# Kernel tuning notes

Measured on AMD Instinct MI355X. Metric: run time of the kernel, lower is better.

The kernel has to match this reference:

```python
import jax, jax.numpy as jnp
import numpy as np

N_NODES = 100000
N_EDGES = 1600000
N_GRAPHS = 1024
HID = 128
FINAL = 128
SPATIAL = 3
NUM_LAYERS = 3
VOCAB = 100


def _linear_params(key, d_in, d_out):
    k1, k2 = jax.random.split(key)
    s = 1.0 / np.sqrt(d_in)
    W = jax.random.uniform(k1, (d_out, d_in), jnp.float32, -s, s)
    b = jax.random.uniform(k2, (d_out,), jnp.float32, -s, s)
    return W, b


def setup_inputs() -> dict:
    key = jax.random.key(0)
    ks = jax.random.split(key, 16)
    z = jax.random.randint(ks[0], (N_NODES,), 0, VOCAB)
    pos = jax.random.normal(ks[1], (N_NODES, SPATIAL), jnp.float32)
    edge_index = jax.random.randint(ks[2], (2, N_EDGES), 0, N_NODES)
    batch = jnp.sort(jax.random.randint(ks[3], (N_NODES,), 0, N_GRAPHS))
    emb_table = jax.random.normal(ks[4], (VOCAB, HID), jnp.float32)
    W_pos, b_pos = _linear_params(ks[5], SPATIAL, HID)
    W_comb, b_comb = _linear_params(ks[6], 2 * HID, HID)
    # GIN: each conv's MLP is Linear(d,d) -> ReLU -> Linear(d,d); all dims 128 here.
    gW1, gb1, gW2, gb2 = [], [], [], []
    for i in range(NUM_LAYERS):
        k = jax.random.fold_in(ks[7], i)
        ka, kb = jax.random.split(k)
        W1, b1 = _linear_params(ka, HID, HID)
        W2, b2 = _linear_params(kb, HID, FINAL if i == NUM_LAYERS - 1 else HID)
        gW1.append(W1); gb1.append(b1); gW2.append(W2); gb2.append(b2)
    gin_W1 = jnp.stack(gW1); gin_b1 = jnp.stack(gb1)
    gin_W2 = jnp.stack(gW2); gin_b2 = jnp.stack(gb2)
    W_p1, b_p1 = _linear_params(ks[8], FINAL, FINAL)
    W_p2, b_p2 = _linear_params(ks[9], FINAL, 1)
    return {
        "z": z, "pos": pos, "edge_index": edge_index, "batch": batch,
        "emb_table": emb_table, "W_pos": W_pos, "b_pos": b_pos,
        "W_comb": W_comb, "b_comb": b_comb,
        "gin_W1": gin_W1, "gin_b1": gin_b1, "gin_W2": gin_W2, "gin_b2": gin_b2,
        "W_p1": W_p1, "b_p1": b_p1, "W_p2": W_p2, "b_p2": b_p2,
    }


def reference(z, pos, edge_index, batch, emb_table, W_pos, b_pos, W_comb, b_comb,
              gin_W1, gin_b1, gin_W2, gin_b2, W_p1, b_p1, W_p2, b_p2):
    src, dst = edge_index[0], edge_index[1]
    # initial node embedding: embed(z) || linear(pos) -> linear -> relu
    atom = emb_table[z]                                   # [N, H]
    pe = pos @ W_pos.T + b_pos                            # [N, H]
    x = jax.nn.relu(jnp.concatenate([atom, pe], axis=-1) @ W_comb.T + b_comb)
    # GIN layers: x' = MLP((1+eps)*x + sum_{j->i} x_j), eps=0; act between convs only
    for i in range(NUM_LAYERS):
        aggr = jax.ops.segment_sum(x[src], dst, num_segments=N_NODES)  # [N, H]
        h = aggr + x
        h = jax.nn.relu(h @ gin_W1[i].T + gin_b1[i])
        x = h @ gin_W2[i].T + gin_b2[i]
        if i < NUM_LAYERS - 1:
            x = jax.nn.relu(x)
    # sum pooling per graph, then predict MLP
    g = jax.ops.segment_sum(x, batch, num_segments=N_GRAPHS)  # [G, F]
    h = jax.nn.relu(g @ W_p1.T + b_p1)
    return h @ W_p2.T + b_p2                              # [G, 1]
```

## Files before the change

kernel.cpp:

```cpp
#include <hip/hip_runtime.h>
#include <hip/hip_bf16.h>

#define HID 128
#define CAP 64

typedef __attribute__((ext_vector_type(8))) short bfrag;
typedef __attribute__((ext_vector_type(4))) float f32x4;

static inline size_t align256(size_t x) { return (x + 255) & ~(size_t)255; }

__device__ __forceinline__ unsigned short f2bf(float f) {
  unsigned int x = __float_as_uint(f);
  unsigned int r = x + 0x7fffu + ((x >> 16) & 1u);
  return (unsigned short)(r >> 16);
}
__device__ __forceinline__ float bflo(unsigned int u) { return __uint_as_float(u << 16); }
__device__ __forceinline__ float bfhi(unsigned int u) { return __uint_as_float(u & 0xffff0000u); }


#define NBK 2048

__global__ __launch_bounds__(256) void k_prep(const int* __restrict__ src,
                                              const int* __restrict__ dst,
                                              int* __restrict__ cnt,
                                              int* __restrict__ bsrc, int E, int N,
                                              const float* __restrict__ W_comb,
                                              const float* __restrict__ gW1,
                                              const float* __restrict__ gW2,
                                              unsigned short* __restrict__ Wcb,
                                              unsigned short* __restrict__ W1b,
                                              unsigned short* __restrict__ W2b,
                                              const int* __restrict__ batch,
                                              int* __restrict__ goff, int G) {
  const int bid = blockIdx.x;
  const int tid = threadIdx.x;
  if (bid < NBK) {
    const int slice = bid & 7;
    const int sidx = bid >> 3;
    const int s_lo = (int)(((long long)slice * N) >> 3);
    const int s_hi = (int)(((long long)(slice + 1) * N) >> 3);
    for (int e = sidx * 256 + tid; e < E; e += (NBK / 8) * 256) {
      int d = dst[e];
      if (d >= s_lo && d < s_hi) {
        int slot = atomicAdd(&cnt[d], 1);
        if (slot < CAP) bsrc[(size_t)d * CAP + slot] = src[e];
      }
    }
  } else if (bid < NBK + 192) {
    int i = (bid - NBK) * 256 + tid;
    if (i < 128 * 256) Wcb[i] = f2bf(W_comb[i]);
    if (i < 3 * 128 * 128) {
      W1b[i] = f2bf(gW1[i]);
      W2b[i] = f2bf(gW2[i]);
    }
  } else {
    int g = (bid - NBK - 192) * 256 + tid;
    if (g <= G) {
      int lo = 0, hi = N;
      while (lo < hi) {
        int mid = (lo + hi) >> 1;
        if (batch[mid] < g) lo = mid + 1; else hi = mid;
      }
      goff[g] = lo;
    }
  }
}


__global__ __launch_bounds__(256, 2) void k_init_mm(const int* __restrict__ z,
                                                    const float* __restrict__ pos,
                                                    const float* __restrict__ emb,
                                                    const float* __restrict__ W_pos,
                                                    const float* __restrict__ b_pos,
                                                    const unsigned short* __restrict__ Wcb,
                                                    const float* __restrict__ bias,
                                                    unsigned short* __restrict__ Y, int n) {
  __shared__ unsigned int sE[32 * 128];
  const int t = threadIdx.x;
  const int w = t >> 6;
  const int l = t & 63;
  const int lr = l & 15;
  const int lk = l >> 4;

  bfrag bfr[2][8];
#pragma unroll
  for (int s = 0; s < 2; ++s)
#pragma unroll
    for (int ks = 0; ks < 8; ++ks)
      bfr[s][ks] = *(const bfrag*)(Wcb + (size_t)(32 * w + 16 * s + lr) * 256 + ks * 32 + lk * 8);
  const float bias0 = bias[32 * w + lr];
  const float bias1 = bias[32 * w + 16 + lr];

  const int m0 = blockIdx.x * 32;
  {
    const int r = t >> 3, i = t & 7;
    int node = m0 + r;
    if (node >= n) node = n - 1;
    const int zz = z[node];
    const float p0 = pos[node * 3 + 0], p1 = pos[node * 3 + 1], p2 = pos[node * 3 + 2];
    const int swz = (r & 7) << 2;
#pragma unroll
    for (int k = 0; k < 16; ++k) {
      const int j = i + k * 8;
      float v0, v1;
      if (j < 64) {
        const float2 ev = *(const float2*)&emb[(size_t)zz * 128 + 2 * j];
        v0 = ev.x; v1 = ev.y;
      } else {
        const int f0 = 2 * j - 128;
        v0 = b_pos[f0] + W_pos[f0 * 3] * p0 + W_pos[f0 * 3 + 1] * p1 + W_pos[f0 * 3 + 2] * p2;
        v1 = b_pos[f0 + 1] + W_pos[f0 * 3 + 3] * p0 + W_pos[f0 * 3 + 4] * p1 +
             W_pos[f0 * 3 + 5] * p2;
      }
      sE[r * 128 + (j ^ swz)] = (unsigned int)f2bf(v0) | ((unsigned int)f2bf(v1) << 16);
    }
  }
  __syncthreads();

  f32x4 acc00 = {0.f, 0.f, 0.f, 0.f}, acc01 = acc00, acc10 = acc00, acc11 = acc00;
#pragma unroll
  for (int mt = 0; mt < 2; ++mt) {
    const int row = 16 * mt + lr;
    const int swz = (row & 7) << 2;
#pragma unroll
    for (int ks = 0; ks < 8; ++ks) {
      const bfrag a = *(const bfrag*)&sE[row * 128 + ((ks * 16 + lk * 4) ^ swz)];
      if (mt == 0) {
        acc00 = __builtin_amdgcn_mfma_f32_16x16x32_bf16(a, bfr[0][ks], acc00, 0, 0, 0);
        acc01 = __builtin_amdgcn_mfma_f32_16x16x32_bf16(a, bfr[1][ks], acc01, 0, 0, 0);
      } else {
        acc10 = __builtin_amdgcn_mfma_f32_16x16x32_bf16(a, bfr[0][ks], acc10, 0, 0, 0);
        acc11 = __builtin_amdgcn_mfma_f32_16x16x32_bf16(a, bfr[1][ks], acc11, 0, 0, 0);
      }
    }
  }

#pragma unroll
  for (int mt = 0; mt < 2; ++mt) {
#pragma unroll
    for (int s = 0; s < 2; ++s) {
      const f32x4 a = mt == 0 ? (s == 0 ? acc00 : acc01) : (s == 0 ? acc10 : acc11);
      const float bb = s == 0 ? bias0 : bias1;
      const int col = 32 * w + 16 * s + lr;
#pragma unroll
      for (int r = 0; r < 4; ++r) {
        const int row = m0 + 16 * mt + 4 * lk + r;
        if (row < n) Y[(size_t)row * HID + col] = f2bf(fmaxf(a[r] + bb, 0.f));
      }
    }
  }
}


__global__ __launch_bounds__(256, 2) void k_ag_mm(const unsigned int* __restrict__ X,
                                                  const int* __restrict__ cnt,
                                                  const int* __restrict__ bsrc,
                                                  const unsigned short* __restrict__ Wb,
                                                  const float* __restrict__ bias,
                                                  unsigned short* __restrict__ Y, int n) {
  __shared__ unsigned int sA[32 * 64];
  const int t = threadIdx.x;
  const int w = t >> 6;
  const int l = t & 63;
  const int lr = l & 15;
  const int lk = l >> 4;

  bfrag bfr[2][4];
#pragma unroll
  for (int s = 0; s < 2; ++s)
#pragma unroll
    for (int ks = 0; ks < 4; ++ks)
      bfr[s][ks] = *(const bfrag*)(Wb + (size_t)(32 * w + 16 * s + lr) * HID + ks * 32 + lk * 8);
  const float bias0 = bias[32 * w + lr];
  const float bias1 = bias[32 * w + 16 + lr];

  const int ntiles = (n + 31) >> 5;
  for (int tile = blockIdx.x; tile < ntiles; tile += gridDim.x) {
    const int m0 = tile * 32;
#pragma unroll
    for (int ri = 0; ri < 8; ++ri) {
      const int row = 8 * w + ri;
      int node = m0 + row;
      if (node >= n) node = n - 1;
      int deg = cnt[node];
      if (deg > CAP) deg = CAP;
      const int eidx = bsrc[(size_t)node * CAP + l];
      const unsigned int u = X[(size_t)node * 64 + l];
      float a0 = bflo(u), a1 = bfhi(u);
      float b0 = 0.f, b1 = 0.f, c0 = 0.f, c1 = 0.f, d0 = 0.f, d1 = 0.f;
      int k = 0;
      for (; k + 3 < deg; k += 4) {
        const int s0 = __shfl(eidx, k), s1 = __shfl(eidx, k + 1);
        const int s2 = __shfl(eidx, k + 2), s3 = __shfl(eidx, k + 3);
        const unsigned int ua = X[(size_t)s0 * 64 + l];
        const unsigned int ub = X[(size_t)s1 * 64 + l];
        const unsigned int uc = X[(size_t)s2 * 64 + l];
        const unsigned int ud = X[(size_t)s3 * 64 + l];
        a0 += bflo(ua); a1 += bfhi(ua);
        b0 += bflo(ub); b1 += bfhi(ub);
        c0 += bflo(uc); c1 += bfhi(uc);
        d0 += bflo(ud); d1 += bfhi(ud);
      }
      for (; k < deg; ++k) {
        const unsigned int ua = X[(size_t)__shfl(eidx, k) * 64 + l];
        a0 += bflo(ua); a1 += bfhi(ua);
      }
      const float r0 = (a0 + b0) + (c0 + d0);
      const float r1 = (a1 + b1) + (c1 + d1);
      sA[row * 64 + (l ^ ((row & 7) << 2))] =
          (unsigned int)f2bf(r0) | ((unsigned int)f2bf(r1) << 16);
    }
    __syncthreads();

    f32x4 acc00 = {0.f, 0.f, 0.f, 0.f}, acc01 = acc00, acc10 = acc00, acc11 = acc00;
#pragma unroll
    for (int mt = 0; mt < 2; ++mt) {
      const int row = 16 * mt + lr;
      const int swz = (row & 7) << 2;
#pragma unroll
      for (int ks = 0; ks < 4; ++ks) {
        const bfrag a = *(const bfrag*)&sA[row * 64 + ((ks * 16 + lk * 4) ^ swz)];
        if (mt == 0) {
          acc00 = __builtin_amdgcn_mfma_f32_16x16x32_bf16(a, bfr[0][ks], acc00, 0, 0, 0);
          acc01 = __builtin_amdgcn_mfma_f32_16x16x32_bf16(a, bfr[1][ks], acc01, 0, 0, 0);
        } else {
          acc10 = __builtin_amdgcn_mfma_f32_16x16x32_bf16(a, bfr[0][ks], acc10, 0, 0, 0);
          acc11 = __builtin_amdgcn_mfma_f32_16x16x32_bf16(a, bfr[1][ks], acc11, 0, 0, 0);
        }
      }
    }

#pragma unroll
    for (int mt = 0; mt < 2; ++mt) {
#pragma unroll
      for (int s = 0; s < 2; ++s) {
        const f32x4 a = mt == 0 ? (s == 0 ? acc00 : acc01) : (s == 0 ? acc10 : acc11);
        const float bb = s == 0 ? bias0 : bias1;
        const int col = 32 * w + 16 * s + lr;
#pragma unroll
        for (int r = 0; r < 4; ++r) {
          const int row = m0 + 16 * mt + 4 * lk + r;
          if (row < n) Y[(size_t)row * HID + col] = f2bf(fmaxf(a[r] + bb, 0.f));
        }
      }
    }
    __syncthreads();
  }
}


template <int RELU>
__global__ __launch_bounds__(256, 2) void k_mm2(const unsigned short* __restrict__ X,
                                                const unsigned short* __restrict__ Wb,
                                                const float* __restrict__ bias,
                                                unsigned short* __restrict__ Y, int M) {
  const int t = threadIdx.x;
  const int w = t >> 6;
  const int l = t & 63;
  const int lr = l & 15;
  const int lk = l >> 4;

  bfrag bfr[2][4];
#pragma unroll
  for (int s = 0; s < 2; ++s)
#pragma unroll
    for (int ks = 0; ks < 4; ++ks)
      bfr[s][ks] = *(const bfrag*)(Wb + (size_t)(32 * w + 16 * s + lr) * HID + ks * 32 + lk * 8);
  const float bias0 = bias[32 * w + lr];
  const float bias1 = bias[32 * w + 16 + lr];

  for (int m0 = blockIdx.x * 32; m0 < M; m0 += gridDim.x * 32) {
    bfrag afr[2][4];
#pragma unroll
    for (int mt = 0; mt < 2; ++mt)
#pragma unroll
      for (int ks = 0; ks < 4; ++ks)
        afr[mt][ks] = *(const bfrag*)(X + (size_t)(m0 + 16 * mt + lr) * HID + ks * 32 + lk * 8);

    f32x4 acc00 = {0.f, 0.f, 0.f, 0.f}, acc01 = acc00, acc10 = acc00, acc11 = acc00;
#pragma unroll
    for (int ks = 0; ks < 4; ++ks) {
      acc00 = __builtin_amdgcn_mfma_f32_16x16x32_bf16(afr[0][ks], bfr[0][ks], acc00, 0, 0, 0);
      acc01 = __builtin_amdgcn_mfma_f32_16x16x32_bf16(afr[0][ks], bfr[1][ks], acc01, 0, 0, 0);
      acc10 = __builtin_amdgcn_mfma_f32_16x16x32_bf16(afr[1][ks], bfr[0][ks], acc10, 0, 0, 0);
      acc11 = __builtin_amdgcn_mfma_f32_16x16x32_bf16(afr[1][ks], bfr[1][ks], acc11, 0, 0, 0);
    }

#pragma unroll
    for (int mt = 0; mt < 2; ++mt) {
#pragma unroll
      for (int s = 0; s < 2; ++s) {
        const f32x4 a = mt == 0 ? (s == 0 ? acc00 : acc01) : (s == 0 ? acc10 : acc11);
        const float bb = s == 0 ? bias0 : bias1;
        const int col = 32 * w + 16 * s + lr;
#pragma unroll
        for (int r = 0; r < 4; ++r) {
          const int row = m0 + 16 * mt + 4 * lk + r;
          float v = a[r] + bb;
          if (RELU) v = fmaxf(v, 0.f);
          if (row < M) Y[(size_t)row * HID + col] = f2bf(v);
        }
      }
    }
  }
}


__global__ __launch_bounds__(128) void k_pool(const unsigned short* __restrict__ X,
                                              const int* __restrict__ goff,
                                              const float* __restrict__ Wp1,
                                              const float* __restrict__ bp1,
                                              const float* __restrict__ Wp2,
                                              const float* __restrict__ bp2,
                                              float* __restrict__ out, int G) {
  __shared__ float sg[HID];
  __shared__ float sred[HID];
  int g = blockIdx.x;
  int f = threadIdx.x;
  int n0 = goff[g], n1 = goff[g + 1];
  float c0 = 0.f, c1 = 0.f, c2 = 0.f, c3 = 0.f;
  int nn = n0;
  for (; nn + 3 < n1; nn += 4) {
    c0 += __uint_as_float((unsigned int)X[(size_t)nn * HID + f] << 16);
    c1 += __uint_as_float((unsigned int)X[(size_t)(nn + 1) * HID + f] << 16);
    c2 += __uint_as_float((unsigned int)X[(size_t)(nn + 2) * HID + f] << 16);
    c3 += __uint_as_float((unsigned int)X[(size_t)(nn + 3) * HID + f] << 16);
  }
  for (; nn < n1; ++nn) c0 += __uint_as_float((unsigned int)X[(size_t)nn * HID + f] << 16);
  sg[f] = (c0 + c1) + (c2 + c3);
  __syncthreads();
  float a0 = 0.f, a1 = 0.f, a2 = 0.f, a3 = 0.f;
#pragma unroll
  for (int k4 = 0; k4 < 32; ++k4) {
    float4 wv = *(const float4*)&Wp1[f * HID + k4 * 4];
    float4 xv = *(const float4*)&sg[k4 * 4];
    a0 += wv.x * xv.x; a1 += wv.y * xv.y; a2 += wv.z * xv.z; a3 += wv.w * xv.w;
  }
  float h = fmaxf(bp1[f] + ((a0 + a1) + (a2 + a3)), 0.f);
  sred[f] = Wp2[f] * h;
  __syncthreads();
  for (int s = 64; s > 0; s >>= 1) {
    if (f < s) sred[f] += sred[f + s];
    __syncthreads();
  }
  if (f == 0) out[g] = sred[0] + bp2[0];
}


extern "C" void kernel_launch(void* const* d_in, const int* in_sizes, int n_in,
                              void* d_out, int out_size, void* d_ws, size_t ws_size,
                              hipStream_t stream) {
  const int*   z      = (const int*)d_in[0];
  const float* pos    = (const float*)d_in[1];
  const int*   ei     = (const int*)d_in[2];
  const int*   batch  = (const int*)d_in[3];
  const float* emb    = (const float*)d_in[4];
  const float* W_pos  = (const float*)d_in[5];
  const float* b_pos  = (const float*)d_in[6];
  const float* W_comb = (const float*)d_in[7];
  const float* b_comb = (const float*)d_in[8];
  const float* gW1    = (const float*)d_in[9];
  const float* gb1    = (const float*)d_in[10];
  const float* gW2    = (const float*)d_in[11];
  const float* gb2    = (const float*)d_in[12];
  const float* Wp1    = (const float*)d_in[13];
  const float* bp1    = (const float*)d_in[14];
  const float* Wp2    = (const float*)d_in[15];
  const float* bp2    = (const float*)d_in[16];
  float* out = (float*)d_out;

  const int N = in_sizes[0];
  const int E = in_sizes[2] / 2;
  const int G = out_size;
  const int* srcp = ei;
  const int* dstp = ei + E;

  char* w = (char*)d_ws;
  unsigned short* Xb  = (unsigned short*)w; w += align256((size_t)N * 128 * 2);
  unsigned short* Hb  = (unsigned short*)w; w += align256((size_t)N * 128 * 2);
  unsigned short* Wcb = (unsigned short*)w; w += align256((size_t)128 * 256 * 2);
  unsigned short* W1b = (unsigned short*)w; w += align256((size_t)3 * 128 * 128 * 2);
  unsigned short* W2b = (unsigned short*)w; w += align256((size_t)3 * 128 * 128 * 2);
  int* cnt  = (int*)w; w += align256((size_t)N * 4);
  int* bsrc = (int*)w; w += align256((size_t)N * CAP * 4);
  int* goff = (int*)w; w += align256((size_t)(G + 1) * 4);

  hipMemsetAsync(cnt, 0, (size_t)N * 4, stream);

  k_prep<<<NBK + 192 + 5, 256, 0, stream>>>(srcp, dstp, cnt, bsrc, E, N,
                                            W_comb, gW1, gW2, Wcb, W1b, W2b,
                                            batch, goff, G);

  k_init_mm<<<(N + 31) / 32, 256, 0, stream>>>(z, pos, emb, W_pos, b_pos, Wcb, b_comb, Xb, N);

  for (int i = 0; i < 3; ++i) {
    k_ag_mm<<<2048, 256, 0, stream>>>((const unsigned int*)Xb, cnt, bsrc,
                                      W1b + (size_t)i * 128 * 128, gb1 + i * 128, Hb, N);
    if (i < 2)
      k_mm2<1><<<1024, 256, 0, stream>>>(Hb, W2b + (size_t)i * 128 * 128, gb2 + i * 128, Xb, N);
    else
      k_mm2<0><<<1024, 256, 0, stream>>>(Hb, W2b + (size_t)i * 128 * 128, gb2 + i * 128, Xb, N);
  }

  k_pool<<<G, HID, 0, stream>>>(Xb, goff, Wp1, bp1, Wp2, bp2, out, G);
}
```

Baseline: 486.5 us.

## Apply W1 before aggregation and fuse each GIN layer into one kernel

Uses linearity so that the first GIN linear (W1) is applied before neighbour aggregation: each node's features are pre-multiplied by the next layer's W1, and the aggregation then sums transformed rows, adds the bias and applies ReLU. Each layer becomes a single kernel that gathers, runs the W2 matmul, then applies the next layer's W1, all through shared memory. This removes the separate k_mm2 launches and their HBM round trip for the hidden activations. The gather loop is also rewritten into an 8-way masked unrolled loop. The cost is an extra matmul in the init kernel and more register and shared-memory pressure. Rounding to bf16 now happens at different points, which slightly changes numerics.

```diff
diff --git a/kernel.cpp b/kernel.cpp
--- a/kernel.cpp
+++ b/kernel.cpp
@@ -3,6 +3,8 @@
 
 #define HID 128
 #define CAP 64
+#define NBK 2048
+#define NBL 1563
 
 typedef __attribute__((ext_vector_type(8))) short bfrag;
 typedef __attribute__((ext_vector_type(4))) float f32x4;
@@ -17,8 +19,6 @@
 __device__ __forceinline__ float bflo(unsigned int u) { return __uint_as_float(u << 16); }
 __device__ __forceinline__ float bfhi(unsigned int u) { return __uint_as_float(u & 0xffff0000u); }
 
-
-#define NBK 2048
 
 __global__ __launch_bounds__(256) void k_prep(const int* __restrict__ src,
                                               const int* __restrict__ dst,
@@ -74,20 +74,25 @@
                                                     const float* __restrict__ b_pos,
                                                     const unsigned short* __restrict__ Wcb,
                                                     const float* __restrict__ bias,
+                                                    const unsigned short* __restrict__ W1n,
                                                     unsigned short* __restrict__ Y, int n) {
   __shared__ unsigned int sE[32 * 128];
+  __shared__ unsigned int sB[32 * 64];
   const int t = threadIdx.x;
-  const int w = t >> 6;
-  const int l = t & 63;
-  const int lr = l & 15;
-  const int lk = l >> 4;
-
-  bfrag bfr[2][8];
+  const int w = t >> 6, l = t & 63, lr = l & 15, lk = l >> 4;
+
+  bfrag wcf[2][8];
 #pragma unroll
   for (int s = 0; s < 2; ++s)
 #pragma unroll
     for (int ks = 0; ks < 8; ++ks)
-      bfr[s][ks] = *(const bfrag*)(Wcb + (size_t)(32 * w + 16 * s + lr) * 256 + ks * 32 + lk * 8);
+      wcf[s][ks] = *(const bfrag*)(Wcb + (size_t)(32 * w + 16 * s + lr) * 256 + ks * 32 + lk * 8);
+  bfrag w1f[2][4];
+#pragma unroll
+  for (int s = 0; s < 2; ++s)
+#pragma unroll
+    for (int ks = 0; ks < 4; ++ks)
+      w1f[s][ks] = *(const bfrag*)(W1n + (size_t)(32 * w + 16 * s + lr) * HID + ks * 32 + lk * 8);
   const float bias0 = bias[32 * w + lr];
   const float bias1 = bias[32 * w + 16 + lr];
 
@@ -126,58 +131,103 @@
     for (int ks = 0; ks < 8; ++ks) {
       const bfrag a = *(const bfrag*)&sE[row * 128 + ((ks * 16 + lk * 4) ^ swz)];
       if (mt == 0) {
-        acc00 = __builtin_amdgcn_mfma_f32_16x16x32_bf16(a, bfr[0][ks], acc00, 0, 0, 0);
-        acc01 = __builtin_amdgcn_mfma_f32_16x16x32_bf16(a, bfr[1][ks], acc01, 0, 0, 0);
+        acc00 = __builtin_amdgcn_mfma_f32_16x16x32_bf16(a, wcf[0][ks], acc00, 0, 0, 0);
+        acc01 = __builtin_amdgcn_mfma_f32_16x16x32_bf16(a, wcf[1][ks], acc01, 0, 0, 0);
       } else {
-        acc10 = __builtin_amdgcn_mfma_f32_16x16x32_bf16(a, bfr[0][ks], acc10, 0, 0, 0);
-        acc11 = __builtin_amdgcn_mfma_f32_16x16x32_bf16(a, bfr[1][ks], acc11, 0, 0, 0);
-      }
-    }
-  }
-
+        acc10 = __builtin_amdgcn_mfma_f32_16x16x32_bf16(a, wcf[0][ks], acc10, 0, 0, 0);
+        acc11 = __builtin_amdgcn_mfma_f32_16x16x32_bf16(a, wcf[1][ks], acc11, 0, 0, 0);
+      }
+    }
+  }
+  {
+    unsigned short* sB16 = (unsigned short*)sB;
+#pragma unroll
+    for (int mt = 0; mt < 2; ++mt) {
+#pragma unroll
+      for (int s = 0; s < 2; ++s) {
+        const f32x4 a = mt == 0 ? (s == 0 ? acc00 : acc01) : (s == 0 ? acc10 : acc11);
+        const float bb = s == 0 ? bias0 : bias1;
+        const int col = 32 * w + 16 * s + lr;
+#pragma unroll
+        for (int r = 0; r < 4; ++r) {
+          const int rowL = 16 * mt + 4 * lk + r;
+          const int cu = (col >> 1) ^ ((rowL & 7) << 2);
+          sB16[rowL * 128 + cu * 2 + (col & 1)] = f2bf(fmaxf(a[r] + bb, 0.f));
+        }
+      }
+    }
+  }
+  __syncthreads();
+
+  f32x4 u00 = {0.f, 0.f, 0.f, 0.f}, u01 = u00, u10 = u00, u11 = u00;
 #pragma unroll
   for (int mt = 0; mt < 2; ++mt) {
+    const int row = 16 * mt + lr;
+    const int swz = (row & 7) << 2;
+#pragma unroll
+    for (int ks = 0; ks < 4; ++ks) {
+      const bfrag a = *(const bfrag*)&sB[row * 64 + ((ks * 16 + lk * 4) ^ swz)];
+      if (mt == 0) {
+        u00 = __builtin_amdgcn_mfma_f32_16x16x32_bf16(a, w1f[0][ks], u00, 0, 0, 0);
+        u01 = __builtin_amdgcn_mfma_f32_16x16x32_bf16(a, w1f[1][ks], u01, 0, 0, 0);
+      } else {
+        u10 = __builtin_amdgcn_mfma_f32_16x16x32_bf16(a, w1f[0][ks], u10, 0, 0, 0);
+        u11 = __builtin_amdgcn_mfma_f32_16x16x32_bf16(a, w1f[1][ks], u11, 0, 0, 0);
+      }
+    }
+  }
+#pragma unroll
+  for (int mt = 0; mt < 2; ++mt) {
 #pragma unroll
     for (int s = 0; s < 2; ++s) {
-      const f32x4 a = mt == 0 ? (s == 0 ? acc00 : acc01) : (s == 0 ? acc10 : acc11);
-      const float bb = s == 0 ? bias0 : bias1;
+      const f32x4 a = mt == 0 ? (s == 0 ? u00 : u01) : (s == 0 ? u10 : u11);
       const int col = 32 * w + 16 * s + lr;
 #pragma unroll
       for (int r = 0; r < 4; ++r) {
         const int row = m0 + 16 * mt + 4 * lk + r;
-        if (row < n) Y[(size_t)row * HID + col] = f2bf(fmaxf(a[r] + bb, 0.f));
-      }
-    }
-  }
-}
-
-
-__global__ __launch_bounds__(256, 2) void k_ag_mm(const unsigned int* __restrict__ X,
+        if (row < n) Y[(size_t)row * HID + col] = f2bf(a[r]);
+      }
+    }
+  }
+}
+
+
+template <int LAST>
+__global__ __launch_bounds__(256, 2) void k_layer(const unsigned int* __restrict__ U,
                                                   const int* __restrict__ cnt,
                                                   const int* __restrict__ bsrc,
-                                                  const unsigned short* __restrict__ Wb,
-                                                  const float* __restrict__ bias,
+                                                  const float* __restrict__ b1,
+                                                  const unsigned short* __restrict__ W2b,
+                                                  const float* __restrict__ b2,
+                                                  const unsigned short* __restrict__ W1n,
                                                   unsigned short* __restrict__ Y, int n) {
   __shared__ unsigned int sA[32 * 64];
+  __shared__ unsigned int sB[32 * 64];
   const int t = threadIdx.x;
-  const int w = t >> 6;
-  const int l = t & 63;
-  const int lr = l & 15;
-  const int lk = l >> 4;
-
-  bfrag bfr[2][4];
+  const int w = t >> 6, l = t & 63, lr = l & 15, lk = l >> 4;
+
+  bfrag w2f[2][4];
 #pragma unroll
   for (int s = 0; s < 2; ++s)
 #pragma unroll
     for (int ks = 0; ks < 4; ++ks)
-      bfr[s][ks] = *(const bfrag*)(Wb + (size_t)(32 * w + 16 * s + lr) * HID + ks * 32 + lk * 8);
-  const float bias0 = bias[32 * w + lr];
-  const float bias1 = bias[32 * w + 16 + lr];
+      w2f[s][ks] = *(const bfrag*)(W2b + (size_t)(32 * w + 16 * s + lr) * HID + ks * 32 + lk * 8);
+  bfrag w1f[2][4];
+  if (!LAST) {
+#pragma unroll
+    for (int s = 0; s < 2; ++s)
+#pragma unroll
+      for (int ks = 0; ks < 4; ++ks)
+        w1f[s][ks] = *(const bfrag*)(W1n + (size_t)(32 * w + 16 * s + lr) * HID + ks * 32 + lk * 8);
+  }
+  const float b2a = b2[32 * w + lr];
+  const float b2b = b2[32 * w + 16 + lr];
+  const float2 b1v = *(const float2*)&b1[2 * l];
 
   const int ntiles = (n + 31) >> 5;
   for (int tile = blockIdx.x; tile < ntiles; tile += gridDim.x) {
     const int m0 = tile * 32;
-#pragma unroll
+#pragma unroll 1
     for (int ri = 0; ri < 8; ++ri) {
       const int row = 8 * w + ri;
       int node = m0 + row;
@@ -185,30 +235,30 @@
       int deg = cnt[node];
       if (deg > CAP) deg = CAP;
       const int eidx = bsrc[(size_t)node * CAP + l];
-      const unsigned int u = X[(size_t)node * 64 + l];
-      float a0 = bflo(u), a1 = bfhi(u);
-      float b0 = 0.f, b1 = 0.f, c0 = 0.f, c1 = 0.f, d0 = 0.f, d1 = 0.f;
-      int k = 0;
-      for (; k + 3 < deg; k += 4) {
-        const int s0 = __shfl(eidx, k), s1 = __shfl(eidx, k + 1);
-        const int s2 = __shfl(eidx, k + 2), s3 = __shfl(eidx, k + 3);
-        const unsigned int ua = X[(size_t)s0 * 64 + l];
-        const unsigned int ub = X[(size_t)s1 * 64 + l];
-        const unsigned int uc = X[(size_t)s2 * 64 + l];
-        const unsigned int ud = X[(size_t)s3 * 64 + l];
-        a0 += bflo(ua); a1 += bfhi(ua);
-        b0 += bflo(ub); b1 += bfhi(ub);
-        c0 += bflo(uc); c1 += bfhi(uc);
-        d0 += bflo(ud); d1 += bfhi(ud);
-      }
-      for (; k < deg; ++k) {
-        const unsigned int ua = X[(size_t)__shfl(eidx, k) * 64 + l];
-        a0 += bflo(ua); a1 += bfhi(ua);
-      }
-      const float r0 = (a0 + b0) + (c0 + d0);
-      const float r1 = (a1 + b1) + (c1 + d1);
+      const unsigned int us = U[(size_t)node * 64 + l];
+      float s0[8], s1[8];
+#pragma unroll
+      for (int jj = 0; jj < 8; ++jj) { s0[jj] = 0.f; s1[jj] = 0.f; }
+      s0[0] = bflo(us); s1[0] = bfhi(us);
+      if (deg > 0) {
+        for (int k = 0; k < deg; k += 8) {
+#pragma unroll
+          for (int jj = 0; jj < 8; ++jj) {
+            const int kk = k + jj;
+            const int lane = kk < deg ? kk : deg - 1;
+            const int sidx = __shfl(eidx, lane);
+            const unsigned int uu = U[(size_t)sidx * 64 + l];
+            const float m = kk < deg ? 1.f : 0.f;
+            s0[jj] += m * bflo(uu);
+            s1[jj] += m * bfhi(uu);
+          }
+        }
+      }
+      const float r0 = ((s0[0] + s0[1]) + (s0[2] + s0[3])) + ((s0[4] + s0[5]) + (s0[6] + s0[7]));
+      const float r1 = ((s1[0] + s1[1]) + (s1[2] + s1[3])) + ((s1[4] + s1[5]) + (s1[6] + s1[7]));
       sA[row * 64 + (l ^ ((row & 7) << 2))] =
-          (unsigned int)f2bf(r0) | ((unsigned int)f2bf(r1) << 16);
+          (unsigned int)f2bf(fmaxf(r0 + b1v.x, 0.f)) |
+          ((unsigned int)f2bf(fmaxf(r1 + b1v.y, 0.f)) << 16);
     }
     __syncthreads();
 
@@ -221,84 +271,76 @@
       for (int ks = 0; ks < 4; ++ks) {
         const bfrag a = *(const bfrag*)&sA[row * 64 + ((ks * 16 + lk * 4) ^ swz)];
         if (mt == 0) {
-          acc00 = __builtin_amdgcn_mfma_f32_16x16x32_bf16(a, bfr[0][ks], acc00, 0, 0, 0);
-          acc01 = __builtin_amdgcn_mfma_f32_16x16x32_bf16(a, bfr[1][ks], acc01, 0, 0, 0);
+          acc00 = __builtin_amdgcn_mfma_f32_16x16x32_bf16(a, w2f[0][ks], acc00, 0, 0, 0);
+          acc01 = __builtin_amdgcn_mfma_f32_16x16x32_bf16(a, w2f[1][ks], acc01, 0, 0, 0);
         } else {
-          acc10 = __builtin_amdgcn_mfma_f32_16x16x32_bf16(a, bfr[0][ks], acc10, 0, 0, 0);
-          acc11 = __builtin_amdgcn_mfma_f32_16x16x32_bf16(a, bfr[1][ks], acc11, 0, 0, 0);
-        }
-      }
-    }
-
-#pragma unroll
-    for (int mt = 0; mt < 2; ++mt) {
-#pragma unroll
-      for (int s = 0; s < 2; ++s) {
-        const f32x4 a = mt == 0 ? (s == 0 ? acc00 : acc01) : (s == 0 ? acc10 : acc11);
-        const float bb = s == 0 ? bias0 : bias1;
-        const int col = 32 * w + 16 * s + lr;
-#pragma unroll
-        for (int r = 0; r < 4; ++r) {
-          const int row = m0 + 16 * mt + 4 * lk + r;
-          if (row < n) Y[(size_t)row * HID + col] = f2bf(fmaxf(a[r] + bb, 0.f));
-        }
-      }
-    }
-    __syncthreads();
-  }
-}
-
-
-template <int RELU>
-__global__ __launch_bounds__(256, 2) void k_mm2(const unsigned short* __restrict__ X,
-                                                const unsigned short* __restrict__ Wb,
-                                                const float* __restrict__ bias,
-                                                unsigned short* __restrict__ Y, int M) {
-  const int t = threadIdx.x;
-  const int w = t >> 6;
-  const int l = t & 63;
-  const int lr = l & 15;
-  const int lk = l >> 4;
-
-  bfrag bfr[2][4];
-#pragma unroll
-  for (int s = 0; s < 2; ++s)
-#pragma unroll
-    for (int ks = 0; ks < 4; ++ks)
-      bfr[s][ks] = *(const bfrag*)(Wb + (size_t)(32 * w + 16 * s + lr) * HID + ks * 32 + lk * 8);
-  const float bias0 = bias[32 * w + lr];
-  const float bias1 = bias[32 * w + 16 + lr];
-
-  for (int m0 = blockIdx.x * 32; m0 < M; m0 += gridDim.x * 32) {
-    bfrag afr[2][4];
-#pragma unroll
-    for (int mt = 0; mt < 2; ++mt)
-#pragma unroll
-      for (int ks = 0; ks < 4; ++ks)
-        afr[mt][ks] = *(const bfrag*)(X + (size_t)(m0 + 16 * mt + lr) * HID + ks * 32 + lk * 8);
-
-    f32x4 acc00 = {0.f, 0.f, 0.f, 0.f}, acc01 = acc00, acc10 = acc00, acc11 = acc00;
-#pragma unroll
-    for (int ks = 0; ks < 4; ++ks) {
-      acc00 = __builtin_amdgcn_mfma_f32_16x16x32_bf16(afr[0][ks], bfr[0][ks], acc00, 0, 0, 0);
-      acc01 = __builtin_amdgcn_mfma_f32_16x16x32_bf16(afr[0][ks], bfr[1][ks], acc01, 0, 0, 0);
-      acc10 = __builtin_amdgcn_mfma_f32_16x16x32_bf16(afr[1][ks], bfr[0][ks], acc10, 0, 0, 0);
-      acc11 = __builtin_amdgcn_mfma_f32_16x16x32_bf16(afr[1][ks], bfr[1][ks], acc11, 0, 0, 0);
-    }
-
-#pragma unroll
-    for (int mt = 0; mt < 2; ++mt) {
-#pragma unroll
-      for (int s = 0; s < 2; ++s) {
-        const f32x4 a = mt == 0 ? (s == 0 ? acc00 : acc01) : (s == 0 ? acc10 : acc11);
-        const float bb = s == 0 ? bias0 : bias1;
-        const int col = 32 * w + 16 * s + lr;
-#pragma unroll
-        for (int r = 0; r < 4; ++r) {
-          const int row = m0 + 16 * mt + 4 * lk + r;
-          float v = a[r] + bb;
-          if (RELU) v = fmaxf(v, 0.f);
-          if (row < M) Y[(size_t)row * HID + col] = f2bf(v);
+          acc10 = __builtin_amdgcn_mfma_f32_16x16x32_bf16(a, w2f[0][ks], acc10, 0, 0, 0);
+          acc11 = __builtin_amdgcn_mfma_f32_16x16x32_bf16(a, w2f[1][ks], acc11, 0, 0, 0);
+        }
+      }
+    }
+    if (LAST) {
+#pragma unroll
+      for (int mt = 0; mt < 2; ++mt) {
+#pragma unroll
+        for (int s = 0; s < 2; ++s) {
+          const f32x4 a = mt == 0 ? (s == 0 ? acc00 : acc01) : (s == 0 ? acc10 : acc11);
+          const float bb = s == 0 ? b2a : b2b;
+          const int col = 32 * w + 16 * s + lr;
+#pragma unroll
+          for (int r = 0; r < 4; ++r) {
+            const int row = m0 + 16 * mt + 4 * lk + r;
+            if (row < n) Y[(size_t)row * HID + col] = f2bf(a[r] + bb);
+          }
+        }
+      }
+      __syncthreads();
+    } else {
+      unsigned short* sB16 = (unsigned short*)sB;
+#pragma unroll
+      for (int mt = 0; mt < 2; ++mt) {
+#pragma unroll
+        for (int s = 0; s < 2; ++s) {
+          const f32x4 a = mt == 0 ? (s == 0 ? acc00 : acc01) : (s == 0 ? acc10 : acc11);
+          const float bb = s == 0 ? b2a : b2b;
+          const int col = 32 * w + 16 * s + lr;
+#pragma unroll
+          for (int r = 0; r < 4; ++r) {
+            const int rowL = 16 * mt + 4 * lk + r;
+            const int cu = (col >> 1) ^ ((rowL & 7) << 2);
+            sB16[rowL * 128 + cu * 2 + (col & 1)] = f2bf(fmaxf(a[r] + bb, 0.f));
+          }
+        }
+      }
+      __syncthreads();
+      f32x4 u00 = {0.f, 0.f, 0.f, 0.f}, u01 = u00, u10 = u00, u11 = u00;
+#pragma unroll
+      for (int mt = 0; mt < 2; ++mt) {
+        const int row = 16 * mt + lr;
+        const int swz = (row & 7) << 2;
+#pragma unroll
+        for (int ks = 0; ks < 4; ++ks) {
+          const bfrag a = *(const bfrag*)&sB[row * 64 + ((ks * 16 + lk * 4) ^ swz)];
+          if (mt == 0) {
+            u00 = __builtin_amdgcn_mfma_f32_16x16x32_bf16(a, w1f[0][ks], u00, 0, 0, 0);
+            u01 = __builtin_amdgcn_mfma_f32_16x16x32_bf16(a, w1f[1][ks], u01, 0, 0, 0);
+          } else {
+            u10 = __builtin_amdgcn_mfma_f32_16x16x32_bf16(a, w1f[0][ks], u10, 0, 0, 0);
+            u11 = __builtin_amdgcn_mfma_f32_16x16x32_bf16(a, w1f[1][ks], u11, 0, 0, 0);
+          }
+        }
+      }
+#pragma unroll
+      for (int mt = 0; mt < 2; ++mt) {
+#pragma unroll
+        for (int s = 0; s < 2; ++s) {
+          const f32x4 a = mt == 0 ? (s == 0 ? u00 : u01) : (s == 0 ? u10 : u11);
+          const int col = 32 * w + 16 * s + lr;
+#pragma unroll
+          for (int r = 0; r < 4; ++r) {
+            const int row = m0 + 16 * mt + 4 * lk + r;
+            if (row < n) Y[(size_t)row * HID + col] = f2bf(a[r]);
+          }
         }
       }
     }
@@ -376,8 +418,8 @@
   const int* dstp = ei + E;
 
   char* w = (char*)d_ws;
-  unsigned short* Xb  = (unsigned short*)w; w += align256((size_t)N * 128 * 2);
-  unsigned short* Hb  = (unsigned short*)w; w += align256((size_t)N * 128 * 2);
+  unsigned short* Ub  = (unsigned short*)w; w += align256((size_t)N * 128 * 2);
+  unsigned short* Vb  = (unsigned short*)w; w += align256((size_t)N * 128 * 2);
   unsigned short* Wcb = (unsigned short*)w; w += align256((size_t)128 * 256 * 2);
   unsigned short* W1b = (unsigned short*)w; w += align256((size_t)3 * 128 * 128 * 2);
   unsigned short* W2b = (unsigned short*)w; w += align256((size_t)3 * 128 * 128 * 2);
@@ -391,16 +433,17 @@
                                             W_comb, gW1, gW2, Wcb, W1b, W2b,
                                             batch, goff, G);
 
-  k_init_mm<<<(N + 31) / 32, 256, 0, stream>>>(z, pos, emb, W_pos, b_pos, Wcb, b_comb, Xb, N);
-
-  for (int i = 0; i < 3; ++i) {
-    k_ag_mm<<<2048, 256, 0, stream>>>((const unsigned int*)Xb, cnt, bsrc,
-                                      W1b + (size_t)i * 128 * 128, gb1 + i * 128, Hb, N);
-    if (i < 2)
-      k_mm2<1><<<1024, 256, 0, stream>>>(Hb, W2b + (size_t)i * 128 * 128, gb2 + i * 128, Xb, N);
-    else
-      k_mm2<0><<<1024, 256, 0, stream>>>(Hb, W2b + (size_t)i * 128 * 128, gb2 + i * 128, Xb, N);
-  }
-
-  k_pool<<<G, HID, 0, stream>>>(Xb, goff, Wp1, bp1, Wp2, bp2, out, G);
-}
+  k_init_mm<<<(N + 31) / 32, 256, 0, stream>>>(z, pos, emb, W_pos, b_pos, Wcb, b_comb,
+                                               W1b, Ub, N);
+
+  k_layer<0><<<NBL, 256, 0, stream>>>((const unsigned int*)Ub, cnt, bsrc, gb1,
+                                      W2b, gb2, W1b + (size_t)1 * 128 * 128, Vb, N);
+  k_layer<0><<<NBL, 256, 0, stream>>>((const unsigned int*)Vb, cnt, bsrc, gb1 + 128,
+                                      W2b + (size_t)1 * 128 * 128, gb2 + 128,
+                                      W1b + (size_t)2 * 128 * 128, Ub, N);
+  k_layer<1><<<NBL, 256, 0, stream>>>((const unsigned int*)Ub, cnt, bsrc, gb1 + 256,
+                                      W2b + (size_t)2 * 128 * 128, gb2 + 256,
+                                      (const unsigned short*)nullptr, Vb, N);
+
+  k_pool<<<G, HID, 0, stream>>>(Vb, goff, Wp1, bp1, Wp2, bp2, out, G);
+}
```

Result: faster. 476.6 us (-2.0%).
